# Performance work log

Hardware: AMD Instinct MI355X
Metric: run time of the kernel (lower is better)

Reference implementation:

```python
import jax, jax.numpy as jnp
import numpy as np
import math
from jax import lax

SQRT_HALF = math.sqrt(0.5)

def _causal_dilated_conv(x, w, b, dilation):
    # x: [B, C, T], w: [O, I, K] (torch layout), causal left padding (K-1)*dilation
    k = w.shape[-1]
    pad = (k - 1) * dilation
    y = lax.conv_general_dilated(
        x, w,
        window_strides=(1,),
        padding=((pad, 0),),
        rhs_dilation=(dilation,),
        dimension_numbers=('NCH', 'OIH', 'NCH'),
    )
    return y + b[None, :, None]


def setup_inputs() -> dict:
    key = jax.random.key(0)
    ks = jax.random.split(key, 9)
    B, C, S, T, K = 8, 512, 256, 8192, 2
    scale = 1.0 / np.sqrt(C * K)
    return {
        'x': jax.random.normal(ks[0], (B, C, T), jnp.float32),
        'filter_w': jax.random.normal(ks[1], (C, C, K), jnp.float32) * scale,
        'filter_b': jax.random.normal(ks[2], (C,), jnp.float32) * scale,
        'gate_w': jax.random.normal(ks[3], (C, C, K), jnp.float32) * scale,
        'gate_b': jax.random.normal(ks[4], (C,), jnp.float32) * scale,
        'res_w': jax.random.normal(ks[5], (C, C), jnp.float32) / np.sqrt(C),
        'res_b': jax.random.normal(ks[6], (C,), jnp.float32) / np.sqrt(C),
        'skip_w': jax.random.normal(ks[7], (S, C), jnp.float32) / np.sqrt(C),
        'skip_b': jax.random.normal(ks[8], (S,), jnp.float32) / np.sqrt(C),
        'dilation': 4,
    }


def reference(x, filter_w, filter_b, gate_w, gate_b, res_w, res_b, skip_w, skip_b, dilation):
    filter_out = jnp.tanh(_causal_dilated_conv(x, filter_w, filter_b, dilation))
    gate_out = jax.nn.sigmoid(_causal_dilated_conv(x, gate_w, gate_b, dilation))
    x_gated = filter_out * gate_out  # [B, C, T]
    # 1x1 convs as channel contractions
    res_out = jnp.einsum('oc,bct->bot', res_w, x_gated) + res_b[None, :, None]
    skip_out = jnp.einsum('sc,bct->bst', skip_w, x_gated) + skip_b[None, :, None]
    return ((x + res_out) * SQRT_HALF, skip_out)
```

## Files before the change

kernel.cpp:

```cpp
#include <hip/hip_runtime.h>
#include <hip/hip_bf16.h>

typedef __attribute__((ext_vector_type(4))) float f32x4;
typedef __attribute__((ext_vector_type(8))) short bf16x8;
typedef unsigned int   u32;
typedef unsigned short u16;

#define DPAD 8
#define B_   8
#define C_   512
#define T_   8192
#define S_   256

#define OFF_WBIG 0u
#define OFF_W2   2097152u
#define OFF_B1   2883584u
#define OFF_B2   2887680u
#define OFF_XT   2891776u
#define OFF_ZT   70066176u

__device__ __forceinline__ u16 f2bf(float f) {
  u32 u = __builtin_bit_cast(u32, f);
  u += 0x7FFFu + ((u >> 16) & 1u);
  return (u16)(u >> 16);
}
__device__ __forceinline__ float sigm_(float x) { return 1.0f / (1.0f + __expf(-x)); }
__device__ __forceinline__ float tanh_(float x) { return 2.0f / (1.0f + __expf(-2.0f * x)) - 1.0f; }

__device__ __forceinline__ void gload_lds16(const void* g, void* l) {
  __builtin_amdgcn_global_load_lds(
      (const __attribute__((address_space(1))) void*)g,
      (__attribute__((address_space(3))) void*)l, 16, 0, 0);
}

__global__ void pack_kernel(const float* __restrict__ fw, const float* __restrict__ fb,
                            const float* __restrict__ gw, const float* __restrict__ gb,
                            const float* __restrict__ rw, const float* __restrict__ rb,
                            const float* __restrict__ sw, const float* __restrict__ sb,
                            u16* __restrict__ Wbig, u16* __restrict__ W2,
                            float* __restrict__ b1, float* __restrict__ b2,
                            u16* __restrict__ Xt)
{
  int idx = blockIdx.x * 256 + threadIdx.x;
  if (idx < 1048576) {
    int row = idx >> 10, k = idx & 1023;
    int i = row >> 1;
    const float* src = (row & 1) ? gw : fw;
    float v = src[((i << 9) + (k & 511)) * 2 + ((k < 512) ? 1 : 0)];
    Wbig[idx] = f2bf(v);
    return;
  }
  idx -= 1048576;
  if (idx < 393216) {
    int r = idx >> 9, k = idx & 511;
    float v = (r < 512) ? rw[(r << 9) + k] : sw[((r - 512) << 9) + k];
    W2[idx] = f2bf(v);
    return;
  }
  idx -= 393216;
  if (idx < 1024) { b1[idx] = (idx & 1) ? gb[idx >> 1] : fb[idx >> 1]; return; }
  idx -= 1024;
  if (idx < 768) { b2[idx] = (idx < 512) ? rb[idx] : sb[idx - 512]; return; }
  idx -= 768;
  if (idx < B_ * DPAD * C_) {
    int b = idx >> 12;
    int rest = idx & 4095;
    Xt[(size_t)b * (T_ + DPAD) * C_ + rest] = 0;
  }
}

__global__ __launch_bounds__(256) void transpose_kernel(const float* __restrict__ x,
                                                        u16* __restrict__ Xt)
{
  __shared__ float tile[64][65];
  int bid = blockIdx.x;
  int ct = bid & 7, tt = (bid >> 3) & 127, b = bid >> 10;
  int w = threadIdx.x >> 6, ln = threadIdx.x & 63;
  const float* xp = x + ((size_t)(b * C_ + ct * 64)) * T_ + tt * 64;
#pragma unroll
  for (int r = 0; r < 16; ++r) {
    int cl = r * 4 + w;
    tile[cl][ln] = xp[(size_t)cl * T_ + ln];
  }
  __syncthreads();
  u16* op = Xt + ((size_t)b * (T_ + DPAD) + DPAD + tt * 64) * C_ + ct * 64;
#pragma unroll
  for (int r = 0; r < 16; ++r) {
    int tl = r * 4 + w;
    op[(size_t)tl * C_ + ln] = f2bf(tile[ln][tl]);
  }
}

__global__ __launch_bounds__(512, 2) void gemm1_kernel(
    const u16* __restrict__ W, const u16* __restrict__ Xt,
    const float* __restrict__ b1, u16* __restrict__ Zt,
    const int* __restrict__ dptr)
{
  __shared__ __align__(16) u16 smem[65536];
  const int dcap = *dptr;
  const int tid = threadIdx.x;
  const int lane = tid & 63, wave = tid >> 6;
  const int wm = wave >> 2, wn = wave & 3;
  const int lp = lane & 15, lg = lane >> 4, lx = lane & 7;

  const int bid = blockIdx.x;
  const int xcd = bid & 7;
  const int idx = bid >> 3;
  const int mt  = idx & 3;
  const int nt  = (xcd << 5) | (idx >> 2);
  const int m0  = mt * 256;
  const int n0g = nt * 256;
  const int b = n0g >> 13, t0 = n0g & (T_ - 1);
  const size_t xtb = (size_t)b * (T_ + DPAD) * C_;

  const int srl = tid >> 3;
  const int skb = tid & 7;
  const int sxk = (skb ^ (srl & 7)) << 3;

  f32x4 acc[8][4];
#pragma unroll
  for (int i = 0; i < 8; ++i)
#pragma unroll
    for (int j = 0; j < 4; ++j) acc[i][j] = (f32x4){0.f, 0.f, 0.f, 0.f};

#define SQA(kt_, dd, q_) do {                                                  \
    const int row_ = (q_) * 64 + srl;                                          \
    gload_lds16(W + (size_t)(m0 + row_) * 1024 + (kt_) * 64 + sxk,             \
                smem + (dd) * 16384 + (q_) * 4096 + tid * 8);                  \
  } while (0)

#define SQB(kt_, dd, q_) do {                                                  \
    const int row_ = (q_) * 64 + srl;                                          \
    const int kg_  = (kt_) * 64 + sxk;                                         \
    const int rsh_ = (kg_ >= 512) ? dcap : 0;                                  \
    gload_lds16(Xt + xtb + (size_t)(DPAD + t0 + row_ - rsh_) * C_ + (kg_ & 511), \
                smem + 32768 + (dd) * 16384 + (q_) * 4096 + tid * 8);          \
  } while (0)

#define LDA_(Ab_, f_, kk_) \
  (*(const bf16x8*)((Ab_) + (size_t)(wm * 128 + (f_) * 16 + lp) * 64 + ((((kk_) * 4 + lg) ^ lx) << 3)))
#define LDB_(Bb_, j_, kk_) \
  (*(const bf16x8*)((Bb_) + (size_t)(wn * 64 + (j_) * 16 + lp) * 64 + ((((kk_) * 4 + lg) ^ lx) << 3)))

#define PH(dd, p_, WTRAIL, STAGES) do {                                        \
    const u16* Ab_ = smem + (dd) * 16384;                                      \
    const u16* Bb_ = smem + 32768 + (dd) * 16384;                              \
    if ((p_) == 0) {                                                           \
      _Pragma("unroll") for (int j_ = 0; j_ < 4; ++j_) {                       \
        bfr[j_][0] = LDB_(Bb_, j_, 0); bfr[j_][1] = LDB_(Bb_, j_, 1);          \
      }                                                                        \
    }                                                                          \
    bf16x8 a00 = LDA_(Ab_, 2 * (p_), 0),     a01 = LDA_(Ab_, 2 * (p_), 1);     \
    bf16x8 a10 = LDA_(Ab_, 2 * (p_) + 1, 0), a11 = LDA_(Ab_, 2 * (p_) + 1, 1); \
    STAGES;                                                                    \
    __builtin_amdgcn_sched_barrier(0);                                         \
    __builtin_amdgcn_s_barrier();                                              \
    asm volatile("s_waitcnt lgkmcnt(0)" ::: "memory");                         \
    __builtin_amdgcn_sched_barrier(0);                                         \
    __builtin_amdgcn_s_setprio(1);                                             \
    _Pragma("unroll") for (int kk_ = 0; kk_ < 2; ++kk_) {                      \
      const bf16x8 aa0_ = kk_ ? a01 : a00;                                     \
      const bf16x8 aa1_ = kk_ ? a11 : a10;                                     \
      _Pragma("unroll") for (int j_ = 0; j_ < 4; ++j_)                         \
        acc[2*(p_)][j_]   = __builtin_amdgcn_mfma_f32_16x16x32_bf16(aa0_, bfr[j_][kk_], acc[2*(p_)][j_],   0, 0, 0); \
      _Pragma("unroll") for (int j_ = 0; j_ < 4; ++j_)                         \
        acc[2*(p_)+1][j_] = __builtin_amdgcn_mfma_f32_16x16x32_bf16(aa1_, bfr[j_][kk_], acc[2*(p_)+1][j_], 0, 0, 0); \
    }                                                                          \
    __builtin_amdgcn_s_setprio(0);                                             \
    WTRAIL;                                                                    \
    __builtin_amdgcn_sched_barrier(0);                                         \
    __builtin_amdgcn_s_barrier();                                              \
  } while (0)

#define VMW(n_) asm volatile("s_waitcnt vmcnt(" #n_ ")" ::: "memory")

  bf16x8 bfr[4][2];

  SQB(0, 0, 0); SQB(0, 0, 1); SQB(0, 0, 2); SQB(0, 0, 3);
  SQA(0, 0, 0); SQA(0, 0, 2); SQA(0, 0, 1); SQA(0, 0, 3);
  VMW(2);
  __builtin_amdgcn_sched_barrier(0);
  __builtin_amdgcn_s_barrier();

  for (int t = 0; t < 15; ++t) {
    const int dd = t & 1, de = dd ^ 1;
    PH(dd, 0,       , { SQB(t + 1, de, 0); SQB(t + 1, de, 1); });
    PH(dd, 1, VMW(4), { SQB(t + 1, de, 2); SQB(t + 1, de, 3); });
    PH(dd, 2,       , { SQA(t + 1, de, 0); SQA(t + 1, de, 2); });
    PH(dd, 3, VMW(2), { SQA(t + 1, de, 1); SQA(t + 1, de, 3); });
  }
  PH(1, 0,       , );
  PH(1, 1, VMW(0), );
  PH(1, 2,       , );
  PH(1, 3,       , );

  const int g = lane >> 4, p = lane & 15;
#pragma unroll
  for (int i = 0; i < 8; ++i) {
    const int R = m0 + wm * 128 + i * 16 + (g << 2);
    const float bi0 = b1[R], bi1 = b1[R + 1], bi2 = b1[R + 2], bi3 = b1[R + 3];
    const int c0 = R >> 1;
#pragma unroll
    for (int j = 0; j < 4; ++j) {
      const int ttc = t0 + wn * 64 + j * 16 + p;
      f32x4 v = acc[i][j];
      float z0 = tanh_(v[0] + bi0) * sigm_(v[1] + bi1);
      float z1 = tanh_(v[2] + bi2) * sigm_(v[3] + bi3);
      u32 pk = (u32)f2bf(z0) | ((u32)f2bf(z1) << 16);
      *(u32*)(Zt + (size_t)(b * T_ + ttc) * C_ + c0) = pk;
    }
  }
#undef SQA
#undef SQB
#undef LDA_
#undef LDB_
#undef PH
#undef VMW
}

__global__ __launch_bounds__(256, 4) void gemm2_kernel(
    const u16* __restrict__ W2, const u16* __restrict__ Zt,
    const float* __restrict__ b2, const float* __restrict__ x,
    float* __restrict__ out)
{
  __shared__ __align__(16) u16 As[128 * 32];
  __shared__ __align__(16) u16 Bs[128 * 32];
  __shared__ __align__(16) float fstall[4 * 1088];
  const int tid = threadIdx.x;
  const int lane = tid & 63, wave = tid >> 6;
  const int wm = wave >> 1, wn = wave & 1;

  const int bid = blockIdx.x;
  const int xcd = bid & 7;
  const int idx = bid >> 3;
  const int mt  = idx % 6;
  const int nt  = (xcd << 6) + idx / 6;
  const int m0 = mt * 128;
  const int n0g = nt * 128;
  const int b = n0g >> 13, t0 = n0g & (T_ - 1);
  const int srow = tid >> 2;
  const int skk  = (tid & 3) * 8;

  f32x4 acc[4][4];
#pragma unroll
  for (int i = 0; i < 4; ++i)
#pragma unroll
    for (int j = 0; j < 4; ++j) acc[i][j] = (f32x4){0.f, 0.f, 0.f, 0.f};

  const int aoff = (wm * 64 + (lane & 15)) * 32 + (lane >> 4) * 8;
  const int boff = (wn * 64 + (lane & 15)) * 32 + (lane >> 4) * 8;
  const size_t ztb = (size_t)b * T_ * C_;

  for (int kc = 0; kc < 16; ++kc) {
    const int k = kc * 32 + skk;
    const u16* gA = W2 + (size_t)(m0 + srow) * 512 + k;
    const u16* gB = Zt + ztb + (size_t)(t0 + srow) * C_ + k;
    gload_lds16(gA,            As + tid * 8);
    gload_lds16(gA + 64 * 512, As + 2048 + tid * 8);
    gload_lds16(gB,            Bs + tid * 8);
    gload_lds16(gB + 64 * C_,  Bs + 2048 + tid * 8);
    asm volatile("s_waitcnt vmcnt(0)" ::: "memory");
    __syncthreads();
    bf16x8 af[4], bfr[4];
#pragma unroll
    for (int i = 0; i < 4; ++i) af[i]  = *(const bf16x8*)(As + aoff + i * 512);
#pragma unroll
    for (int j = 0; j < 4; ++j) bfr[j] = *(const bf16x8*)(Bs + boff + j * 512);
#pragma unroll
    for (int i = 0; i < 4; ++i)
#pragma unroll
      for (int j = 0; j < 4; ++j)
        acc[i][j] = __builtin_amdgcn_mfma_f32_16x16x32_bf16(af[i], bfr[j], acc[i][j], 0, 0, 0);
    __syncthreads();
  }

  float* const fst = fstall + wave * 1088;
  const int g = lane >> 4, p = lane & 15;
  const bool isres = (m0 < 512);

#pragma unroll
  for (int i = 0; i < 4; ++i) {
#pragma unroll
    for (int j = 0; j < 4; ++j)
#pragma unroll
      for (int r = 0; r < 4; ++r)
        fst[(g * 4 + r) * 68 + j * 16 + p] = acc[i][j][r];
#pragma unroll
    for (int q = 0; q < 4; ++q) {
      const int lrow = q * 4 + g;
      const int row = m0 + wm * 64 + i * 16 + lrow;
      const int t = t0 + wn * 64 + p * 4;
      f32x4 v = *(const f32x4*)&fst[lrow * 68 + p * 4];
      const float bias = b2[row];
      f32x4 res;
      if (isres) {
        const size_t o = ((size_t)(b * 512 + row)) * T_ + t;
        f32x4 xv = *(const f32x4*)(x + o);
#pragma unroll
        for (int e = 0; e < 4; ++e)
          res[e] = (xv[e] + v[e] + bias) * 0.70710678118654752f;
        *(f32x4*)(out + o) = res;
      } else {
        const size_t o = (size_t)33554432 + ((size_t)(b * 256 + (row - 512))) * T_ + t;
#pragma unroll
        for (int e = 0; e < 4; ++e)
          res[e] = v[e] + bias;
        *(f32x4*)(out + o) = res;
      }
    }
  }
}

extern "C" void kernel_launch(void* const* d_in, const int* in_sizes, int n_in,
                              void* d_out, int out_size, void* d_ws, size_t ws_size,
                              hipStream_t stream) {
  const float* x  = (const float*)d_in[0];
  const float* fw = (const float*)d_in[1];
  const float* fb = (const float*)d_in[2];
  const float* gw = (const float*)d_in[3];
  const float* gb = (const float*)d_in[4];
  const float* rw = (const float*)d_in[5];
  const float* rb = (const float*)d_in[6];
  const float* sw = (const float*)d_in[7];
  const float* sb = (const float*)d_in[8];
  const int* dil  = (const int*)d_in[9];

  char* ws = (char*)d_ws;
  u16*   Wbig = (u16*)(ws + OFF_WBIG);
  u16*   W2   = (u16*)(ws + OFF_W2);
  float* b1   = (float*)(ws + OFF_B1);
  float* b2   = (float*)(ws + OFF_B2);
  u16*   Xt   = (u16*)(ws + OFF_XT);
  u16*   Zt   = (u16*)(ws + OFF_ZT);
  float* out  = (float*)d_out;

  hipLaunchKernelGGL(pack_kernel, dim3(5767), dim3(256), 0, stream,
                     fw, fb, gw, gb, rw, rb, sw, sb, Wbig, W2, b1, b2, Xt);
  hipLaunchKernelGGL(transpose_kernel, dim3(8192), dim3(256), 0, stream, x, Xt);
  hipLaunchKernelGGL(gemm1_kernel, dim3(1024), dim3(512), 0, stream, Wbig, Xt, b1, Zt, dil);
  hipLaunchKernelGGL(gemm2_kernel, dim3(3072), dim3(256), 0, stream, W2, Zt, b2, x, out);
}
```

Measured before the change: 314.8 us.

## Restructure gemm1 main loop to one barrier per K-tile with register-double-buffered A fragments

Replaces the four-phase loop, which had two barriers per phase, with a single barrier per K-tile. A-fragment LDS reads are double-buffered in registers (aW/aX) so the next phase's reads overlap the current MFMAs, with fine-grained lgkmcnt waits. Global-to-LDS prefetches for the next tile are issued in two bursts, and the loop waits for all of them (vmcnt(0)) at the end of each tile. This cuts barrier overhead but can expose global load latency that was previously hidden by partial vmcnt waits, and it uses more registers.

New measurement: 307.4 us. 2.4% less time.

```diff
diff --git a/kernel.cpp b/kernel.cpp
--- a/kernel.cpp
+++ b/kernel.cpp
@@ -142,62 +142,81 @@
 #define LDB_(Bb_, j_, kk_) \
   (*(const bf16x8*)((Bb_) + (size_t)(wn * 64 + (j_) * 16 + lp) * 64 + ((((kk_) * 4 + lg) ^ lx) << 3)))
 
-#define PH(dd, p_, WTRAIL, STAGES) do {                                        \
-    const u16* Ab_ = smem + (dd) * 16384;                                      \
-    const u16* Bb_ = smem + 32768 + (dd) * 16384;                              \
-    if ((p_) == 0) {                                                           \
-      _Pragma("unroll") for (int j_ = 0; j_ < 4; ++j_) {                       \
-        bfr[j_][0] = LDB_(Bb_, j_, 0); bfr[j_][1] = LDB_(Bb_, j_, 1);          \
-      }                                                                        \
-    }                                                                          \
-    bf16x8 a00 = LDA_(Ab_, 2 * (p_), 0),     a01 = LDA_(Ab_, 2 * (p_), 1);     \
-    bf16x8 a10 = LDA_(Ab_, 2 * (p_) + 1, 0), a11 = LDA_(Ab_, 2 * (p_) + 1, 1); \
-    STAGES;                                                                    \
-    __builtin_amdgcn_sched_barrier(0);                                         \
-    __builtin_amdgcn_s_barrier();                                              \
-    asm volatile("s_waitcnt lgkmcnt(0)" ::: "memory");                         \
-    __builtin_amdgcn_sched_barrier(0);                                         \
+#define READA(a_, p_, Ab_) do {                                                \
+    a_[0] = LDA_(Ab_, 2 * (p_), 0);  a_[1] = LDA_(Ab_, 2 * (p_), 1);           \
+    a_[2] = LDA_(Ab_, 2 * (p_) + 1, 0); a_[3] = LDA_(Ab_, 2 * (p_) + 1, 1);    \
+  } while (0)
+
+#define MFMAPH(a_, p_) do {                                                    \
     __builtin_amdgcn_s_setprio(1);                                             \
     _Pragma("unroll") for (int kk_ = 0; kk_ < 2; ++kk_) {                      \
-      const bf16x8 aa0_ = kk_ ? a01 : a00;                                     \
-      const bf16x8 aa1_ = kk_ ? a11 : a10;                                     \
       _Pragma("unroll") for (int j_ = 0; j_ < 4; ++j_)                         \
-        acc[2*(p_)][j_]   = __builtin_amdgcn_mfma_f32_16x16x32_bf16(aa0_, bfr[j_][kk_], acc[2*(p_)][j_],   0, 0, 0); \
+        acc[2*(p_)][j_]   = __builtin_amdgcn_mfma_f32_16x16x32_bf16(a_[kk_],     bfr[j_][kk_], acc[2*(p_)][j_],   0, 0, 0); \
       _Pragma("unroll") for (int j_ = 0; j_ < 4; ++j_)                         \
-        acc[2*(p_)+1][j_] = __builtin_amdgcn_mfma_f32_16x16x32_bf16(aa1_, bfr[j_][kk_], acc[2*(p_)+1][j_], 0, 0, 0); \
+        acc[2*(p_)+1][j_] = __builtin_amdgcn_mfma_f32_16x16x32_bf16(a_[2 + kk_], bfr[j_][kk_], acc[2*(p_)+1][j_], 0, 0, 0); \
     }                                                                          \
     __builtin_amdgcn_s_setprio(0);                                             \
-    WTRAIL;                                                                    \
-    __builtin_amdgcn_sched_barrier(0);                                         \
-    __builtin_amdgcn_s_barrier();                                              \
   } while (0)
 
-#define VMW(n_) asm volatile("s_waitcnt vmcnt(" #n_ ")" ::: "memory")
+#define LGKM(n_) do { asm volatile("s_waitcnt lgkmcnt(" #n_ ")" ::: "memory"); \
+                      __builtin_amdgcn_sched_barrier(0); } while (0)
+#define VMW(n_)  do { asm volatile("s_waitcnt vmcnt(" #n_ ")" ::: "memory");   \
+                      __builtin_amdgcn_sched_barrier(0); } while (0)
 
   bf16x8 bfr[4][2];
+  bf16x8 aW[4], aX[4];
 
   SQB(0, 0, 0); SQB(0, 0, 1); SQB(0, 0, 2); SQB(0, 0, 3);
-  SQA(0, 0, 0); SQA(0, 0, 2); SQA(0, 0, 1); SQA(0, 0, 3);
-  VMW(2);
-  __builtin_amdgcn_sched_barrier(0);
+  SQA(0, 0, 0); SQA(0, 0, 1); SQA(0, 0, 2); SQA(0, 0, 3);
+  VMW(0);
   __builtin_amdgcn_s_barrier();
 
   for (int t = 0; t < 15; ++t) {
     const int dd = t & 1, de = dd ^ 1;
-    PH(dd, 0,       , { SQB(t + 1, de, 0); SQB(t + 1, de, 1); });
-    PH(dd, 1, VMW(4), { SQB(t + 1, de, 2); SQB(t + 1, de, 3); });
-    PH(dd, 2,       , { SQA(t + 1, de, 0); SQA(t + 1, de, 2); });
-    PH(dd, 3, VMW(2), { SQA(t + 1, de, 1); SQA(t + 1, de, 3); });
-  }
-  PH(1, 0,       , );
-  PH(1, 1, VMW(0), );
-  PH(1, 2,       , );
-  PH(1, 3,       , );
-
-  const int g = lane >> 4, p = lane & 15;
+    const u16* Ab = smem + dd * 16384;
+    const u16* Bb = smem + 32768 + dd * 16384;
+#pragma unroll
+    for (int j = 0; j < 4; ++j) { bfr[j][0] = LDB_(Bb, j, 0); bfr[j][1] = LDB_(Bb, j, 1); }
+    READA(aW, 0, Ab);
+    READA(aX, 1, Ab);
+    LGKM(4);
+    MFMAPH(aW, 0);
+    SQB(t + 1, de, 0); SQB(t + 1, de, 1); SQB(t + 1, de, 2); SQB(t + 1, de, 3);
+    READA(aW, 2, Ab);
+    LGKM(4);
+    MFMAPH(aX, 1);
+    SQA(t + 1, de, 0); SQA(t + 1, de, 1); SQA(t + 1, de, 2); SQA(t + 1, de, 3);
+    READA(aX, 3, Ab);
+    LGKM(4);
+    MFMAPH(aW, 2);
+    LGKM(0);
+    MFMAPH(aX, 3);
+    VMW(0);
+    __builtin_amdgcn_s_barrier();
+  }
+  {
+    const u16* Ab = smem + 16384;
+    const u16* Bb = smem + 49152;
+#pragma unroll
+    for (int j = 0; j < 4; ++j) { bfr[j][0] = LDB_(Bb, j, 0); bfr[j][1] = LDB_(Bb, j, 1); }
+    READA(aW, 0, Ab);
+    READA(aX, 1, Ab);
+    LGKM(4);
+    MFMAPH(aW, 0);
+    READA(aW, 2, Ab);
+    LGKM(4);
+    MFMAPH(aX, 1);
+    READA(aX, 3, Ab);
+    LGKM(4);
+    MFMAPH(aW, 2);
+    LGKM(0);
+    MFMAPH(aX, 3);
+  }
+
+  const int g4 = lane >> 4, p = lane & 15;
 #pragma unroll
   for (int i = 0; i < 8; ++i) {
-    const int R = m0 + wm * 128 + i * 16 + (g << 2);
+    const int R = m0 + wm * 128 + i * 16 + (g4 << 2);
     const float bi0 = b1[R], bi1 = b1[R + 1], bi2 = b1[R + 2], bi3 = b1[R + 3];
     const int c0 = R >> 1;
 #pragma unroll
@@ -214,7 +233,9 @@
 #undef SQB
 #undef LDA_
 #undef LDB_
-#undef PH
+#undef READA
+#undef MFMAPH
+#undef LGKM
 #undef VMW
 }
 
```
